# Kernel optimization log

Measured on AMD Instinct MI355X. Metric: run time of the kernel, lower is better.

Reference implementation:

```python
import jax, jax.numpy as jnp
import numpy as np

TOP_K = 8
SCALE = 2.5  # routed_scaling_factor


def setup_inputs() -> dict:
    key = jax.random.key(0)
    k1, k2, k3 = jax.random.split(key, 3)
    x = jax.random.normal(k1, (4, 4096, 4096), dtype=jnp.float32)
    weight = jax.random.normal(k2, (256, 4096), dtype=jnp.float32) * 0.02  # [n_experts, hidden]
    bias = jax.random.normal(k3, (256,), dtype=jnp.float32) * 0.01  # e_score_correction_bias
    return {"x": x, "weight": weight, "bias": bias}


def reference(x, weight, bias):
    # x: [B, S, H] -> flatten to tokens
    t = x.reshape(-1, x.shape[-1])                      # [T, H]
    logits = jnp.einsum('th,eh->te', t, weight)         # gate linear, [T, E]
    scores = jax.nn.sigmoid(logits)
    scores_for_choice = scores + bias[None, :]          # bias-corrected scores
    topk_weight, topk_idx = jax.lax.top_k(scores_for_choice, TOP_K)  # [T, K]
    denom = jnp.sum(topk_weight, axis=-1, keepdims=True) + 1e-20
    topk_weight = (topk_weight / denom) * SCALE
    return topk_idx, topk_weight
```

## Files before the change

### kernel.cpp

```cpp
#include <hip/hip_runtime.h>
#include <hip/hip_bf16.h>
#include <math.h>


using bf16x8  = __attribute__((ext_vector_type(8))) short;
using f32x4   = __attribute__((ext_vector_type(4))) float;
using short4v = __attribute__((ext_vector_type(4))) short;

constexpr int E_EXPERTS = 256;
constexpr int KDIM      = 4096;
constexpr int TOPK      = 8;
constexpr float SCALE   = 2.5f;

constexpr int BM = 64, BN = 128, BK = 64, NT = 256;
constexpr int NSTEP = KDIM / BK;

__device__ __forceinline__ void load_lds16(const short* g, short* l) {
    auto gp = (const __attribute__((address_space(1))) short*)g;
    auto lp = (__attribute__((address_space(3))) short*)(uintptr_t)l;
    __builtin_amdgcn_global_load_lds(gp, lp, 16, 0, 0);
}

__device__ __forceinline__ void split1(float x, short& h1, short& h2, short& h3) {
    unsigned u = __float_as_uint(x);
    h1 = (short)(u >> 16);
    float r1 = x - __uint_as_float(u & 0xFFFF0000u);
    unsigned u1 = __float_as_uint(r1);
    h2 = (short)(u1 >> 16);
    float r2 = r1 - __uint_as_float(u1 & 0xFFFF0000u);
    h3 = (short)(__float_as_uint(r2) >> 16);
}

__global__ void wsplit_kernel(const float* __restrict__ W, short* __restrict__ W1,
                              short* __restrict__ W2, short* __restrict__ W3) {
    int i = blockIdx.x * 256 + threadIdx.x;
    float4 w = ((const float4*)W)[i];
    short4v s1, s2, s3;
    short a, b, c;
    split1(w.x, a, b, c); s1.x = a; s2.x = b; s3.x = c;
    split1(w.y, a, b, c); s1.y = a; s2.y = b; s3.y = c;
    split1(w.z, a, b, c); s1.z = a; s2.z = b; s3.z = c;
    split1(w.w, a, b, c); s1.w = a; s2.w = b; s3.w = c;
    ((short4v*)W1)[i] = s1;
    ((short4v*)W2)[i] = s2;
    ((short4v*)W3)[i] = s3;
}

__global__ __launch_bounds__(NT, 2) void gate_gemm(
    const float* __restrict__ X,
    const short* __restrict__ W1, const short* __restrict__ W2, const short* __restrict__ W3,
    const float* __restrict__ Bias, float* __restrict__ S) {
    __shared__ short lds[36864];

    const int tid  = threadIdx.x;
    const int lane = tid & 63;
    const int wave = tid >> 6;
    const int wm   = wave >> 1;
    const int wn   = wave & 1;

    const int p       = blockIdx.x;
    const int cpx     = gridDim.x >> 3;
    const int logical = (p & 7) * cpx + (p >> 3);
    const int tok0 = (logical >> 1) * BM;
    const int e0   = (logical & 1) * BN;

    const int ar0 = tid >> 3;
    const int ag  = (tid & 7) ^ (ar0 & 7);
    const float* xr0 = X + (size_t)(tok0 + ar0) * KDIM + ag * 8;
    const float* xr1 = xr0 + (size_t)32 * KDIM;

    const int bsl = (lane & 7) ^ (lane >> 3);

    f32x4 acc[2][4];
#pragma unroll
    for (int i = 0; i < 2; ++i)
#pragma unroll
        for (int j = 0; j < 4; ++j) acc[i][j] = f32x4{0.f, 0.f, 0.f, 0.f};

    for (int ks = 0; ks < NSTEP; ++ks) {
        const int k0 = ks * BK;

        float4 a0 = *(const float4*)(xr0 + k0);
        float4 a1 = *(const float4*)(xr0 + k0 + 4);
        float4 b0 = *(const float4*)(xr1 + k0);
        float4 b1 = *(const float4*)(xr1 + k0 + 4);

#pragma unroll
        for (int lev = 0; lev < 3; ++lev) {
            const short* wl = (lev == 0) ? W1 : ((lev == 1) ? W2 : W3);
#pragma unroll
            for (int h = 0; h < 4; ++h) {
                const int e = h * 32 + wave * 8 + (lane >> 3);
                load_lds16(wl + (size_t)(e0 + e) * KDIM + k0 + bsl * 8,
                           &lds[12288 + lev * 8192 + h * 2048 + wave * 512]);
            }
        }

        bf16x8 p1, p2, p3, q1, q2, q3;
        {
            float v[8] = {a0.x, a0.y, a0.z, a0.w, a1.x, a1.y, a1.z, a1.w};
#pragma unroll
            for (int j = 0; j < 8; ++j) {
                short h1, h2, h3; split1(v[j], h1, h2, h3);
                p1[j] = h1; p2[j] = h2; p3[j] = h3;
            }
        }
        {
            float v[8] = {b0.x, b0.y, b0.z, b0.w, b1.x, b1.y, b1.z, b1.w};
#pragma unroll
            for (int j = 0; j < 8; ++j) {
                short h1, h2, h3; split1(v[j], h1, h2, h3);
                q1[j] = h1; q2[j] = h2; q3[j] = h3;
            }
        }
        *(bf16x8*)&lds[0 * 4096 + tid * 8]        = p1;
        *(bf16x8*)&lds[1 * 4096 + tid * 8]        = p2;
        *(bf16x8*)&lds[2 * 4096 + tid * 8]        = p3;
        *(bf16x8*)&lds[0 * 4096 + 2048 + tid * 8] = q1;
        *(bf16x8*)&lds[1 * 4096 + 2048 + tid * 8] = q2;
        *(bf16x8*)&lds[2 * 4096 + 2048 + tid * 8] = q3;

        __syncthreads();

#pragma unroll
        for (int ksub = 0; ksub < 2; ++ksub) {
            const int slot = (ksub * 4 + (lane >> 4)) ^ (lane & 7);
            bf16x8 af[2][3];
#pragma unroll
            for (int mf = 0; mf < 2; ++mf) {
                const int r = wm * 32 + mf * 16 + (lane & 15);
#pragma unroll
                for (int lev = 0; lev < 3; ++lev)
                    af[mf][lev] = *(const bf16x8*)&lds[lev * 4096 + r * 64 + slot * 8];
            }
            bf16x8 bfr[4][3];
#pragma unroll
            for (int nf = 0; nf < 4; ++nf) {
                const int e = wn * 64 + nf * 16 + (lane & 15);
#pragma unroll
                for (int lev = 0; lev < 3; ++lev)
                    bfr[nf][lev] = *(const bf16x8*)&lds[12288 + lev * 8192 + e * 64 + slot * 8];
            }
#pragma unroll
            for (int mf = 0; mf < 2; ++mf)
#pragma unroll
                for (int nf = 0; nf < 4; ++nf) {
                    f32x4 c = acc[mf][nf];
                    c = __builtin_amdgcn_mfma_f32_16x16x32_bf16(af[mf][0], bfr[nf][0], c, 0, 0, 0);
                    c = __builtin_amdgcn_mfma_f32_16x16x32_bf16(af[mf][0], bfr[nf][1], c, 0, 0, 0);
                    c = __builtin_amdgcn_mfma_f32_16x16x32_bf16(af[mf][1], bfr[nf][0], c, 0, 0, 0);
                    c = __builtin_amdgcn_mfma_f32_16x16x32_bf16(af[mf][1], bfr[nf][1], c, 0, 0, 0);
                    c = __builtin_amdgcn_mfma_f32_16x16x32_bf16(af[mf][0], bfr[nf][2], c, 0, 0, 0);
                    c = __builtin_amdgcn_mfma_f32_16x16x32_bf16(af[mf][2], bfr[nf][0], c, 0, 0, 0);
                    acc[mf][nf] = c;
                }
        }
        __syncthreads();
    }

#pragma unroll
    for (int mf = 0; mf < 2; ++mf)
#pragma unroll
        for (int nf = 0; nf < 4; ++nf) {
            const int ec = e0 + wn * 64 + nf * 16 + (lane & 15);
            const float bv = Bias[ec];
#pragma unroll
            for (int v = 0; v < 4; ++v) {
                const int tr = tok0 + wm * 32 + mf * 16 + (lane >> 4) * 4 + v;
                const float logit = acc[mf][nf][v];
                S[(size_t)tr * E_EXPERTS + ec] = 1.0f / (1.0f + expf(-logit)) + bv;
            }
        }
}

__global__ __launch_bounds__(256) void gate_topk(
    const float* __restrict__ S, float* __restrict__ outIdx,
    float* __restrict__ outW, int T) {
    const int wave = threadIdx.x >> 6;
    const int lane = threadIdx.x & 63;
    const int t    = blockIdx.x * 4 + wave;
    if (t >= T) return;

    const float* row = S + (size_t)t * E_EXPERTS;
    float v[4];
    int   idx[4];
#pragma unroll
    for (int j = 0; j < 4; ++j) {
        idx[j] = lane + 64 * j;
        v[j]   = row[idx[j]];
    }

    float tv[8];
    int   ti[8];
#pragma unroll
    for (int k = 0; k < TOPK; ++k) {
        float bv = v[0];
        int   bi = idx[0];
#pragma unroll
        for (int j = 1; j < 4; ++j)
            if (v[j] > bv) { bv = v[j]; bi = idx[j]; }
#pragma unroll
        for (int off = 1; off < 64; off <<= 1) {
            float ov = __shfl_xor(bv, off);
            int   oi = __shfl_xor(bi, off);
            if (ov > bv || (ov == bv && oi < bi)) { bv = ov; bi = oi; }
        }
        tv[k] = bv;
        ti[k] = bi;
#pragma unroll
        for (int j = 0; j < 4; ++j)
            if (idx[j] == bi) v[j] = -INFINITY;
    }

    float denom = 0.0f;
#pragma unroll
    for (int k = 0; k < TOPK; ++k) denom += tv[k];
    denom += 1e-20f;

#pragma unroll
    for (int k = 0; k < TOPK; ++k) {
        if (lane == k) {
            outIdx[(size_t)t * TOPK + k] = (float)ti[k];
            outW[(size_t)t * TOPK + k]   = (tv[k] / denom) * SCALE;
        }
    }
}

extern "C" void kernel_launch(void* const* d_in, const int* in_sizes, int n_in,
                              void* d_out, int out_size, void* d_ws, size_t ws_size,
                              hipStream_t stream) {
    const float* x    = (const float*)d_in[0];
    const float* w    = (const float*)d_in[1];
    const float* bias = (const float*)d_in[2];

    const int T = in_sizes[0] / KDIM;

    float* S  = (float*)d_ws;
    short* W1 = (short*)((char*)d_ws + (size_t)T * E_EXPERTS * 4);
    short* W2 = W1 + (size_t)E_EXPERTS * KDIM;
    short* W3 = W2 + (size_t)E_EXPERTS * KDIM;

    float* outIdx = (float*)d_out;
    float* outW   = outIdx + (size_t)T * TOPK;

    wsplit_kernel<<<(E_EXPERTS * KDIM / 4) / 256, 256, 0, stream>>>(w, W1, W2, W3);
    gate_gemm<<<(T / BM) * (E_EXPERTS / BN), NT, 0, stream>>>(x, W1, W2, W3, bias, S);
    gate_topk<<<T / 4, 256, 0, stream>>>(S, outIdx, outW, T);
}
```

Before: 204.0 us.

## Fuse gate GEMM with top-k and double-buffer LDS over full expert width

Each block now computes all 256 experts for 64 tokens with 512 threads, so the X tile is read once instead of twice. The top-k selection runs from a shared-memory score tile, which removes the global score buffer and the separate top-k launch. The K loop is double-buffered with BK reduced to 32, and the global load of the next tile overlaps the MFMA work on the current one. The cost is larger LDS use per block (about 120 KB), which may limit occupancy to one block per CU despite the launch bound of 2.

```diff
diff --git a/kernel.cpp b/kernel.cpp
--- a/kernel.cpp
+++ b/kernel.cpp
@@ -3,17 +3,18 @@
 #include <math.h>
 
 
-using bf16x8  = __attribute__((ext_vector_type(8))) short;
-using f32x4   = __attribute__((ext_vector_type(4))) float;
-using short4v = __attribute__((ext_vector_type(4))) short;
+using bf16x4 = __attribute__((ext_vector_type(4))) short;
+using bf16x8 = __attribute__((ext_vector_type(8))) short;
+using f32x4  = __attribute__((ext_vector_type(4))) float;
 
 constexpr int E_EXPERTS = 256;
 constexpr int KDIM      = 4096;
 constexpr int TOPK      = 8;
 constexpr float SCALE   = 2.5f;
 
-constexpr int BM = 64, BN = 128, BK = 64, NT = 256;
+constexpr int BM = 64, BK = 32, NT = 512;
 constexpr int NSTEP = KDIM / BK;
+constexpr int BUFS  = 30720;
 
 __device__ __forceinline__ void load_lds16(const short* g, short* l) {
     auto gp = (const __attribute__((address_space(1))) short*)g;
@@ -35,41 +36,78 @@
                               short* __restrict__ W2, short* __restrict__ W3) {
     int i = blockIdx.x * 256 + threadIdx.x;
     float4 w = ((const float4*)W)[i];
-    short4v s1, s2, s3;
+    bf16x4 s1, s2, s3;
     short a, b, c;
     split1(w.x, a, b, c); s1.x = a; s2.x = b; s3.x = c;
     split1(w.y, a, b, c); s1.y = a; s2.y = b; s3.y = c;
     split1(w.z, a, b, c); s1.z = a; s2.z = b; s3.z = c;
     split1(w.w, a, b, c); s1.w = a; s2.w = b; s3.w = c;
-    ((short4v*)W1)[i] = s1;
-    ((short4v*)W2)[i] = s2;
-    ((short4v*)W3)[i] = s3;
-}
-
-__global__ __launch_bounds__(NT, 2) void gate_gemm(
+    ((bf16x4*)W1)[i] = s1;
+    ((bf16x4*)W2)[i] = s2;
+    ((bf16x4*)W3)[i] = s3;
+}
+
+__global__ __launch_bounds__(NT, 2) void gate_fused(
     const float* __restrict__ X,
     const short* __restrict__ W1, const short* __restrict__ W2, const short* __restrict__ W3,
-    const float* __restrict__ Bias, float* __restrict__ S) {
-    __shared__ short lds[36864];
+    const float* __restrict__ Bias,
+    float* __restrict__ outIdx, float* __restrict__ outW) {
+    __shared__ short lds[2 * BUFS];
 
     const int tid  = threadIdx.x;
     const int lane = tid & 63;
-    const int wave = tid >> 6;
-    const int wm   = wave >> 1;
-    const int wn   = wave & 1;
-
-    const int p       = blockIdx.x;
-    const int cpx     = gridDim.x >> 3;
-    const int logical = (p & 7) * cpx + (p >> 3);
-    const int tok0 = (logical >> 1) * BM;
-    const int e0   = (logical & 1) * BN;
-
-    const int ar0 = tid >> 3;
-    const int ag  = (tid & 7) ^ (ar0 & 7);
-    const float* xr0 = X + (size_t)(tok0 + ar0) * KDIM + ag * 8;
-    const float* xr1 = xr0 + (size_t)32 * KDIM;
-
-    const int bsl = (lane & 7) ^ (lane >> 3);
+    const int w    = tid >> 6;
+    const int wm   = w >> 2;
+    const int wn   = w & 3;
+    const int tok0 = blockIdx.x * BM;
+
+    const int ar = tid >> 3;
+    const int aq = tid & 7;
+    const int ag = aq >> 1, ah = aq & 1;
+    const float* xp = X + (size_t)(tok0 + ar) * KDIM + aq * 4;
+    const int aoff = (ag << 9) + ((ar ^ (ag << 1)) << 3) + (ah << 2);
+
+    const short* wl0 = W1; const short* wl1 = W2; const short* wl2 = W3;
+    int brow[2], bg[2];
+    {
+        int c0 = tid;        bg[0] = c0 >> 8; brow[0] = (c0 & 255) ^ (bg[0] << 1);
+        int c1 = 512 + tid;  bg[1] = c1 >> 8; brow[1] = (c1 & 255) ^ (bg[1] << 1);
+    }
+
+    const int g = lane >> 4;
+    int aro[2], bro[4];
+#pragma unroll
+    for (int mf = 0; mf < 2; ++mf) {
+        int r = wm * 32 + mf * 16 + (lane & 15);
+        aro[mf] = (g << 9) + ((r ^ (g << 1)) << 3);
+    }
+#pragma unroll
+    for (int nf = 0; nf < 4; ++nf) {
+        int e = wn * 64 + nf * 16 + (lane & 15);
+        bro[nf] = (g << 11) + ((e ^ (g << 1)) << 3);
+    }
+
+    auto stageB = [&](short* buf, int k0) {
+#pragma unroll
+        for (int lev = 0; lev < 3; ++lev) {
+            const short* src = (lev == 0) ? wl0 : ((lev == 1) ? wl1 : wl2);
+            short* dst = buf + 6144 + lev * 8192;
+            load_lds16(src + (size_t)brow[0] * KDIM + k0 + (bg[0] << 3), dst + (size_t)tid * 8);
+            load_lds16(src + (size_t)brow[1] * KDIM + k0 + (bg[1] << 3), dst + (size_t)(512 + tid) * 8);
+        }
+    };
+
+    auto writeA = [&](short* buf, float4 a) {
+        bf16x4 s1, s2, s3;
+        short h1, h2, h3;
+        split1(a.x, h1, h2, h3); s1.x = h1; s2.x = h2; s3.x = h3;
+        split1(a.y, h1, h2, h3); s1.y = h1; s2.y = h2; s3.y = h3;
+        split1(a.z, h1, h2, h3); s1.z = h1; s2.z = h2; s3.z = h3;
+        split1(a.w, h1, h2, h3); s1.w = h1; s2.w = h2; s3.w = h3;
+        *(bf16x4*)&buf[0 * 2048 + aoff] = s1;
+        *(bf16x4*)&buf[1 * 2048 + aoff] = s2;
+        *(bf16x4*)&buf[2 * 2048 + aoff] = s3;
+    };
 
     f32x4 acc[2][4];
 #pragma unroll
@@ -77,151 +115,105 @@
 #pragma unroll
         for (int j = 0; j < 4; ++j) acc[i][j] = f32x4{0.f, 0.f, 0.f, 0.f};
 
-    for (int ks = 0; ks < NSTEP; ++ks) {
-        const int k0 = ks * BK;
-
-        float4 a0 = *(const float4*)(xr0 + k0);
-        float4 a1 = *(const float4*)(xr0 + k0 + 4);
-        float4 b0 = *(const float4*)(xr1 + k0);
-        float4 b1 = *(const float4*)(xr1 + k0 + 4);
-
-#pragma unroll
-        for (int lev = 0; lev < 3; ++lev) {
-            const short* wl = (lev == 0) ? W1 : ((lev == 1) ? W2 : W3);
-#pragma unroll
-            for (int h = 0; h < 4; ++h) {
-                const int e = h * 32 + wave * 8 + (lane >> 3);
-                load_lds16(wl + (size_t)(e0 + e) * KDIM + k0 + bsl * 8,
-                           &lds[12288 + lev * 8192 + h * 2048 + wave * 512]);
-            }
-        }
-
-        bf16x8 p1, p2, p3, q1, q2, q3;
-        {
-            float v[8] = {a0.x, a0.y, a0.z, a0.w, a1.x, a1.y, a1.z, a1.w};
-#pragma unroll
-            for (int j = 0; j < 8; ++j) {
-                short h1, h2, h3; split1(v[j], h1, h2, h3);
-                p1[j] = h1; p2[j] = h2; p3[j] = h3;
-            }
-        }
-        {
-            float v[8] = {b0.x, b0.y, b0.z, b0.w, b1.x, b1.y, b1.z, b1.w};
-#pragma unroll
-            for (int j = 0; j < 8; ++j) {
-                short h1, h2, h3; split1(v[j], h1, h2, h3);
-                q1[j] = h1; q2[j] = h2; q3[j] = h3;
-            }
-        }
-        *(bf16x8*)&lds[0 * 4096 + tid * 8]        = p1;
-        *(bf16x8*)&lds[1 * 4096 + tid * 8]        = p2;
-        *(bf16x8*)&lds[2 * 4096 + tid * 8]        = p3;
-        *(bf16x8*)&lds[0 * 4096 + 2048 + tid * 8] = q1;
-        *(bf16x8*)&lds[1 * 4096 + 2048 + tid * 8] = q2;
-        *(bf16x8*)&lds[2 * 4096 + 2048 + tid * 8] = q3;
-
+    auto compute = [&](const short* buf) {
+        bf16x8 af[2][3], bfr[4][3];
+#pragma unroll
+        for (int mf = 0; mf < 2; ++mf)
+#pragma unroll
+            for (int lev = 0; lev < 3; ++lev)
+                af[mf][lev] = *(const bf16x8*)&buf[lev * 2048 + aro[mf]];
+#pragma unroll
+        for (int nf = 0; nf < 4; ++nf)
+#pragma unroll
+            for (int lev = 0; lev < 3; ++lev)
+                bfr[nf][lev] = *(const bf16x8*)&buf[6144 + lev * 8192 + bro[nf]];
+#pragma unroll
+        for (int mf = 0; mf < 2; ++mf)
+#pragma unroll
+            for (int nf = 0; nf < 4; ++nf) {
+                f32x4 c = acc[mf][nf];
+                c = __builtin_amdgcn_mfma_f32_16x16x32_bf16(af[mf][0], bfr[nf][0], c, 0, 0, 0);
+                c = __builtin_amdgcn_mfma_f32_16x16x32_bf16(af[mf][0], bfr[nf][1], c, 0, 0, 0);
+                c = __builtin_amdgcn_mfma_f32_16x16x32_bf16(af[mf][1], bfr[nf][0], c, 0, 0, 0);
+                c = __builtin_amdgcn_mfma_f32_16x16x32_bf16(af[mf][1], bfr[nf][1], c, 0, 0, 0);
+                c = __builtin_amdgcn_mfma_f32_16x16x32_bf16(af[mf][0], bfr[nf][2], c, 0, 0, 0);
+                c = __builtin_amdgcn_mfma_f32_16x16x32_bf16(af[mf][2], bfr[nf][0], c, 0, 0, 0);
+                acc[mf][nf] = c;
+            }
+    };
+
+    stageB(lds, 0);
+    writeA(lds, *(const float4*)xp);
+    __syncthreads();
+
+    int buf = 0;
+    for (int ks = 0; ks < NSTEP - 1; ++ks) {
+        short* cur = lds + buf * BUFS;
+        short* nxt = lds + (buf ^ 1) * BUFS;
+        float4 an = *(const float4*)(xp + (size_t)(ks + 1) * BK);
+        stageB(nxt, (ks + 1) * BK);
+        compute(cur);
+        writeA(nxt, an);
         __syncthreads();
-
-#pragma unroll
-        for (int ksub = 0; ksub < 2; ++ksub) {
-            const int slot = (ksub * 4 + (lane >> 4)) ^ (lane & 7);
-            bf16x8 af[2][3];
-#pragma unroll
-            for (int mf = 0; mf < 2; ++mf) {
-                const int r = wm * 32 + mf * 16 + (lane & 15);
-#pragma unroll
-                for (int lev = 0; lev < 3; ++lev)
-                    af[mf][lev] = *(const bf16x8*)&lds[lev * 4096 + r * 64 + slot * 8];
-            }
-            bf16x8 bfr[4][3];
-#pragma unroll
-            for (int nf = 0; nf < 4; ++nf) {
-                const int e = wn * 64 + nf * 16 + (lane & 15);
-#pragma unroll
-                for (int lev = 0; lev < 3; ++lev)
-                    bfr[nf][lev] = *(const bf16x8*)&lds[12288 + lev * 8192 + e * 64 + slot * 8];
-            }
-#pragma unroll
-            for (int mf = 0; mf < 2; ++mf)
-#pragma unroll
-                for (int nf = 0; nf < 4; ++nf) {
-                    f32x4 c = acc[mf][nf];
-                    c = __builtin_amdgcn_mfma_f32_16x16x32_bf16(af[mf][0], bfr[nf][0], c, 0, 0, 0);
-                    c = __builtin_amdgcn_mfma_f32_16x16x32_bf16(af[mf][0], bfr[nf][1], c, 0, 0, 0);
-                    c = __builtin_amdgcn_mfma_f32_16x16x32_bf16(af[mf][1], bfr[nf][0], c, 0, 0, 0);
-                    c = __builtin_amdgcn_mfma_f32_16x16x32_bf16(af[mf][1], bfr[nf][1], c, 0, 0, 0);
-                    c = __builtin_amdgcn_mfma_f32_16x16x32_bf16(af[mf][0], bfr[nf][2], c, 0, 0, 0);
-                    c = __builtin_amdgcn_mfma_f32_16x16x32_bf16(af[mf][2], bfr[nf][0], c, 0, 0, 0);
-                    acc[mf][nf] = c;
-                }
-        }
-        __syncthreads();
-    }
-
+        buf ^= 1;
+    }
+    compute(lds + buf * BUFS);
+    __syncthreads();
+
+    float* Sl = (float*)lds;
 #pragma unroll
     for (int mf = 0; mf < 2; ++mf)
 #pragma unroll
         for (int nf = 0; nf < 4; ++nf) {
-            const int ec = e0 + wn * 64 + nf * 16 + (lane & 15);
+            const int ec = wn * 64 + nf * 16 + (lane & 15);
             const float bv = Bias[ec];
 #pragma unroll
             for (int v = 0; v < 4; ++v) {
-                const int tr = tok0 + wm * 32 + mf * 16 + (lane >> 4) * 4 + v;
-                const float logit = acc[mf][nf][v];
-                S[(size_t)tr * E_EXPERTS + ec] = 1.0f / (1.0f + expf(-logit)) + bv;
-            }
-        }
-}
-
-__global__ __launch_bounds__(256) void gate_topk(
-    const float* __restrict__ S, float* __restrict__ outIdx,
-    float* __restrict__ outW, int T) {
-    const int wave = threadIdx.x >> 6;
-    const int lane = threadIdx.x & 63;
-    const int t    = blockIdx.x * 4 + wave;
-    if (t >= T) return;
-
-    const float* row = S + (size_t)t * E_EXPERTS;
-    float v[4];
-    int   idx[4];
-#pragma unroll
-    for (int j = 0; j < 4; ++j) {
-        idx[j] = lane + 64 * j;
-        v[j]   = row[idx[j]];
-    }
-
-    float tv[8];
-    int   ti[8];
-#pragma unroll
-    for (int k = 0; k < TOPK; ++k) {
-        float bv = v[0];
-        int   bi = idx[0];
-#pragma unroll
-        for (int j = 1; j < 4; ++j)
-            if (v[j] > bv) { bv = v[j]; bi = idx[j]; }
-#pragma unroll
-        for (int off = 1; off < 64; off <<= 1) {
-            float ov = __shfl_xor(bv, off);
-            int   oi = __shfl_xor(bi, off);
-            if (ov > bv || (ov == bv && oi < bi)) { bv = ov; bi = oi; }
-        }
-        tv[k] = bv;
-        ti[k] = bi;
-#pragma unroll
-        for (int j = 0; j < 4; ++j)
-            if (idx[j] == bi) v[j] = -INFINITY;
-    }
-
-    float denom = 0.0f;
-#pragma unroll
-    for (int k = 0; k < TOPK; ++k) denom += tv[k];
-    denom += 1e-20f;
-
-#pragma unroll
-    for (int k = 0; k < TOPK; ++k) {
-        if (lane == k) {
-            outIdx[(size_t)t * TOPK + k] = (float)ti[k];
-            outW[(size_t)t * TOPK + k]   = (tv[k] / denom) * SCALE;
+                const int tr = wm * 32 + mf * 16 + (lane >> 4) * 4 + v;
+                Sl[tr * 260 + ec] = 1.0f / (1.0f + expf(-acc[mf][nf][v])) + bv;
+            }
+        }
+    __syncthreads();
+
+    for (int tt = w * 8; tt < w * 8 + 8; ++tt) {
+        float v[4];
+        int   idx[4];
+#pragma unroll
+        for (int j = 0; j < 4; ++j) {
+            idx[j] = lane + 64 * j;
+            v[j]   = Sl[tt * 260 + idx[j]];
+        }
+        float tv[TOPK];
+        int   ti[TOPK];
+#pragma unroll
+        for (int k = 0; k < TOPK; ++k) {
+            float bv = v[0];
+            int   bi = idx[0];
+#pragma unroll
+            for (int j = 1; j < 4; ++j)
+                if (v[j] > bv) { bv = v[j]; bi = idx[j]; }
+#pragma unroll
+            for (int off = 1; off < 64; off <<= 1) {
+                float ov = __shfl_xor(bv, off);
+                int   oi = __shfl_xor(bi, off);
+                if (ov > bv || (ov == bv && oi < bi)) { bv = ov; bi = oi; }
+            }
+            tv[k] = bv;
+            ti[k] = bi;
+#pragma unroll
+            for (int j = 0; j < 4; ++j)
+                if (idx[j] == bi) v[j] = -INFINITY;
+        }
+        float denom = 0.0f;
+#pragma unroll
+        for (int k = 0; k < TOPK; ++k) denom += tv[k];
+        denom += 1e-20f;
+#pragma unroll
+        for (int k = 0; k < TOPK; ++k) {
+            if (lane == k) {
+                outIdx[(size_t)(tok0 + tt) * TOPK + k] = (float)ti[k];
+                outW[(size_t)(tok0 + tt) * TOPK + k]   = (tv[k] / denom) * SCALE;
+            }
         }
     }
 }
@@ -235,8 +227,7 @@
 
     const int T = in_sizes[0] / KDIM;
 
-    float* S  = (float*)d_ws;
-    short* W1 = (short*)((char*)d_ws + (size_t)T * E_EXPERTS * 4);
+    short* W1 = (short*)d_ws;
     short* W2 = W1 + (size_t)E_EXPERTS * KDIM;
     short* W3 = W2 + (size_t)E_EXPERTS * KDIM;
 
@@ -244,6 +235,5 @@
     float* outW   = outIdx + (size_t)T * TOPK;
 
     wsplit_kernel<<<(E_EXPERTS * KDIM / 4) / 256, 256, 0, stream>>>(w, W1, W2, W3);
-    gate_gemm<<<(T / BM) * (E_EXPERTS / BN), NT, 0, stream>>>(x, W1, W2, W3, bias, S);
-    gate_topk<<<T / 4, 256, 0, stream>>>(S, outIdx, outW, T);
-}
+    gate_fused<<<T / BM, NT, 0, stream>>>(x, W1, W2, W3, bias, outIdx, outW);
+}
```

Measured after the change: 407.6 us. 99.8% more time.
